# Kernel tuning notes

Hardware: AMD Instinct MI355X
Metric: run time of the kernel (lower is better)

## Reference

```python
import jax, jax.numpy as jnp
import numpy as np

N = 40000   # nodes
E = 640000  # edges (avg degree 16)
D = 128     # feature dim (in_features == out_features)
ALPHA = 0.2 # LeakyReLU negative slope


def setup_inputs() -> dict:
    key = jax.random.key(0)
    ks = jax.random.split(key, 12)
    s = 1.0 / np.sqrt(D)
    return {
        "h":     jax.random.normal(ks[0], (N, D), jnp.float32),
        "src":   jax.random.randint(ks[1], (E,), 0, N, jnp.int32),
        "dst":   jax.random.randint(ks[2], (E,), 0, N, jnp.int32),
        "W":     jax.random.normal(ks[3], (D, D), jnp.float32) * s,
        "b_W":   jnp.zeros((D,), jnp.float32),
        "a_src": jax.random.normal(ks[4], (D,), jnp.float32) * s,
        "a_dst": jax.random.normal(ks[5], (D,), jnp.float32) * s,
        "a_b":   jnp.zeros((1,), jnp.float32),
        "res_W": jax.random.normal(ks[6], (D, D), jnp.float32) * s,
        "res_b": jnp.zeros((D,), jnp.float32),
        "Wi":    jax.random.normal(ks[7], (3 * D, D), jnp.float32) * s,
        "Wh_g":  jax.random.normal(ks[8], (3 * D, D), jnp.float32) * s,
        "bi":    jnp.zeros((3 * D,), jnp.float32),
        "bh":    jnp.zeros((3 * D,), jnp.float32),
    }


def reference(h, src, dst, W, b_W, a_src, a_dst, a_b, res_W, res_b, Wi, Wh_g, bi, bh):
    # --- GAT layer: Wh = W h ---
    Wh = h @ W.T + b_W                                  # [N, D]
    # edge attention: a([Wh_src || Wh_dst]) == Wh_src@a_src + Wh_dst@a_dst + a_b
    s_s = Wh @ a_src                                    # [N]
    s_d = Wh @ a_dst                                    # [N]
    e = jax.nn.leaky_relu(s_s[src] + s_d[dst] + a_b[0], ALPHA)  # [E]
    # segment softmax over incoming edges of each destination node
    m = jax.ops.segment_max(e, dst, num_segments=N)
    m = jnp.where(jnp.isfinite(m), m, 0.0)
    ex = jnp.exp(e - m[dst])                            # [E]
    denom = jax.ops.segment_sum(ex, dst, num_segments=N)
    attn = ex / jnp.where(denom > 0, denom, 1.0)[dst]   # [E]
    # weighted neighbor aggregation (scatter-add on dst)
    h_prime = jax.ops.segment_sum(attn[:, None] * Wh[src], dst, num_segments=N)  # [N, D]
    # residual connection (res=True)
    h_prime = h_prime + h @ res_W.T + res_b
    # --- GRU cell: input = h_prime, hidden = h ---
    gi = h_prime @ Wi.T + bi                            # [N, 3D]
    gh = h @ Wh_g.T + bh                                # [N, 3D]
    i_r, i_z, i_n = jnp.split(gi, 3, axis=-1)
    h_r, h_z, h_n = jnp.split(gh, 3, axis=-1)
    r = jax.nn.sigmoid(i_r + h_r)
    z = jax.nn.sigmoid(i_z + h_z)
    n = jnp.tanh(i_n + r * h_n)
    return (1.0 - z) * n + z * h                        # [N, D]
```

## Files before the change

### kernel.cpp

```cpp
#include <hip/hip_runtime.h>
#include <math.h>

#define NLALPHA 0.2f
#define LOG2E 1.4426950408889634f
#define RT 10
#define SLAB 64
#define EPT 4
#define EPB (256 * EPT)

typedef __attribute__((ext_vector_type(8))) short bf16x8;
typedef __attribute__((ext_vector_type(4))) float f32x4;

static __device__ __forceinline__ float fexp(float x) {
    return __builtin_amdgcn_exp2f(x * LOG2E);
}
static __device__ __forceinline__ float fsigmoid(float x) {
    return __builtin_amdgcn_rcpf(1.f + __builtin_amdgcn_exp2f(-LOG2E * x));
}
static __device__ __forceinline__ float ftanh(float x) {
    return 1.f - 2.f * __builtin_amdgcn_rcpf(1.f + __builtin_amdgcn_exp2f(2.f * LOG2E * x));
}
static __device__ __forceinline__ unsigned short f2bf(float f) {
    unsigned int u = __float_as_uint(f);
    return (unsigned short)((u + 0x7fffu + ((u >> 16) & 1u)) >> 16);
}
static __device__ __forceinline__ float bf2f(unsigned short b) {
    return __uint_as_float(((unsigned int)b) << 16);
}
static __device__ __forceinline__ void keep_alive(bf16x8& v) {
    uint4* q = (uint4*)&v;
    asm volatile("" : "+v"(q->x), "+v"(q->y), "+v"(q->z), "+v"(q->w));
}
static __device__ __forceinline__ void place_edges(const int* __restrict__ dstv,
    const int* __restrict__ srcv, int* __restrict__ cnt, int* __restrict__ slab,
    int blk, int i0, int iEnd)
{
    const int base = i0 + blk * EPB + threadIdx.x;
    int d[EPT], s[EPT], pp[EPT];
    bool v[EPT];
#pragma unroll
    for (int u = 0; u < EPT; ++u) {
        int i = base + u * 256;
        v[u] = i < iEnd;
        if (v[u]) { d[u] = dstv[i]; s[u] = srcv[i]; }
    }
#pragma unroll
    for (int u = 0; u < EPT; ++u)
        if (v[u]) pp[u] = atomicAdd(&cnt[d[u]], 1);
#pragma unroll
    for (int u = 0; u < EPT; ++u)
        if (v[u]) slab[d[u] * SLAB + pp[u]] = s[u];
}

__global__ __launch_bounds__(256) void k_zero(int* __restrict__ cnt,
    const float* __restrict__ W, const float* __restrict__ a_src,
    const float* __restrict__ a_dst, const float* __restrict__ b_W,
    float* __restrict__ va, float* __restrict__ cc, int n, int gZero)
{
    const int b = blockIdx.x;
    if (b < gZero) {
        int i = b * 256 + threadIdx.x;
        if (i < n) cnt[i] = 0;
        return;
    }
    const int k = threadIdx.x;
    float cs = 0.f, cd = 0.f;
    if (k < 128) {
        float ss = 0.f, dd = 0.f;
        for (int j = 0; j < 128; ++j) {
            float w = W[j * 128 + k];
            ss = fmaf(w, a_src[j], ss);
            dd = fmaf(w, a_dst[j], dd);
        }
        va[k] = ss;
        va[128 + k] = dd;
        cs = b_W[k] * a_src[k];
        cd = b_W[k] * a_dst[k];
    }
#pragma unroll
    for (int o = 32; o; o >>= 1) { cs += __shfl_down(cs, o); cd += __shfl_down(cd, o); }
    __shared__ float sh[8];
    if ((k & 63) == 0) { sh[(k >> 6) * 2] = cs; sh[(k >> 6) * 2 + 1] = cd; }
    __syncthreads();
    if (k == 0) {
        cc[0] = sh[0] + sh[2] + sh[4] + sh[6];
        cc[1] = sh[1] + sh[3] + sh[5] + sh[7];
    }
}

__global__ __launch_bounds__(256) void k_prep_place(const float* __restrict__ h,
    const float* __restrict__ W, const float* __restrict__ res_W,
    const float* __restrict__ b_W, const float* __restrict__ res_b,
    const float* __restrict__ Wi, const float* __restrict__ Whg,
    const int* __restrict__ dstv, const int* __restrict__ srcv,
    const float* __restrict__ va, const float* __restrict__ cc,
    unsigned short* __restrict__ h_bf, unsigned short* __restrict__ Wcat,
    unsigned short* __restrict__ Wi_bf, unsigned short* __restrict__ Whg_bf,
    float* __restrict__ bias_cat, float* __restrict__ s_s, float* __restrict__ s_d,
    int* __restrict__ cnt, int* __restrict__ slab, int n, int e1, int gPrep)
{
    const int b = blockIdx.x;
    if (b < gPrep) {
        int i = b * 256 + threadIdx.x;
        int t = threadIdx.x;
        if (i < n * 16) {
            float4 v0 = ((const float4*)h)[2 * i];
            float4 v1 = ((const float4*)h)[2 * i + 1];
            uint4 o;
            o.x = (unsigned int)f2bf(v0.x) | ((unsigned int)f2bf(v0.y) << 16);
            o.y = (unsigned int)f2bf(v0.z) | ((unsigned int)f2bf(v0.w) << 16);
            o.z = (unsigned int)f2bf(v1.x) | ((unsigned int)f2bf(v1.y) << 16);
            o.w = (unsigned int)f2bf(v1.z) | ((unsigned int)f2bf(v1.w) << 16);
            ((uint4*)h_bf)[i] = o;
            const float* vs = va + (t & 15) * 8;
            const float* vd = vs + 128;
            float ps = v0.x*vs[0] + v0.y*vs[1] + v0.z*vs[2] + v0.w*vs[3]
                     + v1.x*vs[4] + v1.y*vs[5] + v1.z*vs[6] + v1.w*vs[7];
            float pd = v0.x*vd[0] + v0.y*vd[1] + v0.z*vd[2] + v0.w*vd[3]
                     + v1.x*vd[4] + v1.y*vd[5] + v1.z*vd[6] + v1.w*vd[7];
#pragma unroll
            for (int o2 = 1; o2 < 16; o2 <<= 1) {
                ps += __shfl_xor(ps, o2);
                pd += __shfl_xor(pd, o2);
            }
            if ((t & 15) == 0) {
                int row = i >> 4;
                s_s[row] = ps + cc[0];
                s_d[row] = pd + cc[1];
            }
        }
        if (i < 32768) Wcat[i] = f2bf(i < 16384 ? W[i] : res_W[i - 16384]);
        if (i < 49152) { Wi_bf[i] = f2bf(Wi[i]); Whg_bf[i] = f2bf(Whg[i]); }
        if (i < 256) bias_cat[i] = (i < 128) ? b_W[i] : res_b[i - 128];
    } else {
        place_edges(dstv, srcv, cnt, slab, b - gPrep, 0, e1);
    }
}

__global__ __launch_bounds__(256, 1) void k_whres_place(
    const unsigned short* __restrict__ h_bf,
    const unsigned short* __restrict__ Wcat, const float* __restrict__ bias_cat,
    unsigned short* __restrict__ Wh, unsigned short* __restrict__ hres,
    const int* __restrict__ dstv, const int* __restrict__ srcv,
    int* __restrict__ cnt, int* __restrict__ slab,
    int n, int e1, int e, int rowBlocks, int gWhres)
{
    const int b = blockIdx.x;
    if (b >= gWhres) {
        place_edges(dstv, srcv, cnt, slab, b - gWhres, e1, e);
        return;
    }
    const int bx = b % rowBlocks;
    const int by = b / rowBlocks;
    const int t = threadIdx.x;
    const int w = t >> 6, l = t & 63;
    const int lr = l & 15, kq = l >> 4, kg = kq * 8;
    const int jc = by * 64 + w * 16 + lr;
    bf16x8 bw[4];
#pragma unroll
    for (int ks = 0; ks < 4; ++ks) {
        bw[ks] = *(const bf16x8*)(Wcat + (size_t)jc * 128 + ks * 32 + kg);
        keep_alive(bw[ks]);
    }
    const float bj = bias_cat[jc];
    unsigned short* dstBase = (jc < 128) ? (Wh + jc) : (hres + (jc - 128));

    int row0 = bx * (16 * RT);
    bf16x8 ac[4];
    {
        const unsigned short* Ap = h_bf + (size_t)min(row0 + lr, n - 1) * 128 + kg;
#pragma unroll
        for (int ks = 0; ks < 4; ++ks) ac[ks] = *(const bf16x8*)(Ap + ks * 32);
    }
    for (int rt = 0; rt < RT && row0 < n; ++rt) {
        const int nrow = row0 + 16;
        bf16x8 an[4];
        if (rt + 1 < RT && nrow < n) {
            const unsigned short* Ap = h_bf + (size_t)min(nrow + lr, n - 1) * 128 + kg;
#pragma unroll
            for (int ks = 0; ks < 4; ++ks) an[ks] = *(const bf16x8*)(Ap + ks * 32);
        }
        f32x4 acc = {};
        acc = __builtin_amdgcn_mfma_f32_16x16x32_bf16(ac[0], bw[0], acc, 0, 0, 0);
        acc = __builtin_amdgcn_mfma_f32_16x16x32_bf16(ac[1], bw[1], acc, 0, 0, 0);
        acc = __builtin_amdgcn_mfma_f32_16x16x32_bf16(ac[2], bw[2], acc, 0, 0, 0);
        acc = __builtin_amdgcn_mfma_f32_16x16x32_bf16(ac[3], bw[3], acc, 0, 0, 0);
#pragma unroll
        for (int r = 0; r < 4; ++r) {
            int row = row0 + kq * 4 + r;
            if (row < n) dstBase[(size_t)row * 128] = f2bf(acc[r] + bj);
        }
#pragma unroll
        for (int ks = 0; ks < 4; ++ks) ac[ks] = an[ks];
        row0 = nrow;
    }
}

__global__ __launch_bounds__(256) void k_attn(const int* __restrict__ cnt,
    const int* __restrict__ slab, const float* __restrict__ s_s,
    const float* __restrict__ s_d, const float* __restrict__ a_b,
    const unsigned short* __restrict__ Wh, const unsigned short* __restrict__ hres,
    unsigned short* __restrict__ hp, int n)
{
    const int node = (int)((blockIdx.x * 256u + threadIdx.x) >> 6);
    const int l = threadIdx.x & 63;
    if (node >= n) return;
    const int lo = node * SLAB;
    const int deg = cnt[node];
    const float sdn = s_d[node] + a_b[0];
    const int g = l >> 4;
    const int c = l & 15;

    float sv = 0.f;
    int ssrc = 0;
    float den = 0.f;
    if (l < deg) {
        int s = slab[lo + l];
        float ev = s_s[s] + sdn;
        ev = ev > 0.f ? ev : NLALPHA * ev;
        sv = fexp(ev);
        ssrc = s;
        den = sv;
    }
#pragma unroll
    for (int o = 32; o; o >>= 1) den += __shfl_xor(den, o);
    const float dinv = __builtin_amdgcn_rcpf(den > 0.f ? den : 1.f);

    float acc[8] = {};
    for (int q = 0; q < deg; q += 4) {
        int eix = q + g;
        bool valid = eix < deg;
        int eic = valid ? eix : (deg - 1);
        float ex = __shfl(sv, eic);
        int s = __shfl(ssrc, eic);
        float wgt = valid ? ex * dinv : 0.f;
        uint4 v = *(const uint4*)(Wh + (size_t)s * 128 + c * 8);
        acc[0] = fmaf(wgt, bf2f((unsigned short)(v.x & 0xffff)), acc[0]);
        acc[1] = fmaf(wgt, bf2f((unsigned short)(v.x >> 16)), acc[1]);
        acc[2] = fmaf(wgt, bf2f((unsigned short)(v.y & 0xffff)), acc[2]);
        acc[3] = fmaf(wgt, bf2f((unsigned short)(v.y >> 16)), acc[3]);
        acc[4] = fmaf(wgt, bf2f((unsigned short)(v.z & 0xffff)), acc[4]);
        acc[5] = fmaf(wgt, bf2f((unsigned short)(v.z >> 16)), acc[5]);
        acc[6] = fmaf(wgt, bf2f((unsigned short)(v.w & 0xffff)), acc[6]);
        acc[7] = fmaf(wgt, bf2f((unsigned short)(v.w >> 16)), acc[7]);
    }
#pragma unroll
    for (int k = 0; k < 8; ++k) {
        acc[k] += __shfl_xor(acc[k], 16);
        acc[k] += __shfl_xor(acc[k], 32);
    }
    if (l < 16) {
        uint4 hv = *(const uint4*)(hres + (size_t)node * 128 + l * 8);
        uint4 o;
        o.x = (unsigned int)f2bf(acc[0] + bf2f((unsigned short)(hv.x & 0xffff)))
            | ((unsigned int)f2bf(acc[1] + bf2f((unsigned short)(hv.x >> 16))) << 16);
        o.y = (unsigned int)f2bf(acc[2] + bf2f((unsigned short)(hv.y & 0xffff)))
            | ((unsigned int)f2bf(acc[3] + bf2f((unsigned short)(hv.y >> 16))) << 16);
        o.z = (unsigned int)f2bf(acc[4] + bf2f((unsigned short)(hv.z & 0xffff)))
            | ((unsigned int)f2bf(acc[5] + bf2f((unsigned short)(hv.z >> 16))) << 16);
        o.w = (unsigned int)f2bf(acc[6] + bf2f((unsigned short)(hv.w & 0xffff)))
            | ((unsigned int)f2bf(acc[7] + bf2f((unsigned short)(hv.w >> 16))) << 16);
        *(uint4*)(hp + (size_t)node * 128 + l * 8) = o;
    }
}

__global__ __launch_bounds__(256, 1) void k_gru(const unsigned short* __restrict__ hp_bf,
    const unsigned short* __restrict__ h_bf, const unsigned short* __restrict__ Wi_bf,
    const unsigned short* __restrict__ Whg_bf, const float* __restrict__ bi,
    const float* __restrict__ bh, float* __restrict__ out, int n)
{
    const int t = threadIdx.x;
    const int w = t >> 6, l = t & 63;
    const int lr = l & 15, kq = l >> 4, kg = kq * 8;
    const int c = blockIdx.y * 64 + w * 16 + lr;

    bf16x8 bwi[3][4], bwh[3][4];
#pragma unroll
    for (int g = 0; g < 3; ++g)
#pragma unroll
        for (int ks = 0; ks < 4; ++ks) {
            bwi[g][ks] = *(const bf16x8*)(Wi_bf  + (size_t)(g * 128 + c) * 128 + ks * 32 + kg);
            bwh[g][ks] = *(const bf16x8*)(Whg_bf + (size_t)(g * 128 + c) * 128 + ks * 32 + kg);
        }
    const float biR = bi[c],       bhR = bh[c];
    const float biZ = bi[128 + c], bhZ = bh[128 + c];
    const float biN = bi[256 + c], bhN = bh[256 + c];

    int row0 = blockIdx.x * (16 * RT);
    bf16x8 aPc[4], aHc[4];
    float hvc[4];
    {
        size_t rbase = (size_t)min(row0 + lr, n - 1) * 128 + kg;
#pragma unroll
        for (int ks = 0; ks < 4; ++ks) {
            aPc[ks] = *(const bf16x8*)(hp_bf + rbase + ks * 32);
            aHc[ks] = *(const bf16x8*)(h_bf + rbase + ks * 32);
        }
#pragma unroll
        for (int r = 0; r < 4; ++r)
            hvc[r] = bf2f(h_bf[(size_t)min(row0 + kq * 4 + r, n - 1) * 128 + c]);
    }
    for (int rt = 0; rt < RT && row0 < n; ++rt) {
        const int nrow = row0 + 16;
        bf16x8 aPn[4], aHn[4];
        float hvn[4];
        if (rt + 1 < RT && nrow < n) {
            size_t rbase = (size_t)min(nrow + lr, n - 1) * 128 + kg;
#pragma unroll
            for (int ks = 0; ks < 4; ++ks) {
                aPn[ks] = *(const bf16x8*)(hp_bf + rbase + ks * 32);
                aHn[ks] = *(const bf16x8*)(h_bf + rbase + ks * 32);
            }
#pragma unroll
            for (int r = 0; r < 4; ++r)
                hvn[r] = bf2f(h_bf[(size_t)min(nrow + kq * 4 + r, n - 1) * 128 + c]);
        }

        f32x4 giR = {}, giZ = {}, giN = {}, ghR = {}, ghZ = {}, ghN = {};
#pragma unroll
        for (int ks = 0; ks < 4; ++ks) {
            giR = __builtin_amdgcn_mfma_f32_16x16x32_bf16(aPc[ks], bwi[0][ks], giR, 0, 0, 0);
            ghR = __builtin_amdgcn_mfma_f32_16x16x32_bf16(aHc[ks], bwh[0][ks], ghR, 0, 0, 0);
            giZ = __builtin_amdgcn_mfma_f32_16x16x32_bf16(aPc[ks], bwi[1][ks], giZ, 0, 0, 0);
            ghZ = __builtin_amdgcn_mfma_f32_16x16x32_bf16(aHc[ks], bwh[1][ks], ghZ, 0, 0, 0);
            giN = __builtin_amdgcn_mfma_f32_16x16x32_bf16(aPc[ks], bwi[2][ks], giN, 0, 0, 0);
            ghN = __builtin_amdgcn_mfma_f32_16x16x32_bf16(aHc[ks], bwh[2][ks], ghN, 0, 0, 0);
        }
#pragma unroll
        for (int r = 0; r < 4; ++r) {
            int row = row0 + kq * 4 + r;
            if (row < n) {
                float rg = fsigmoid(giR[r] + biR + ghR[r] + bhR);
                float zg = fsigmoid(giZ[r] + biZ + ghZ[r] + bhZ);
                float ng = ftanh(giN[r] + biN + rg * (ghN[r] + bhN));
                out[(size_t)row * 128 + c] = (1.f - zg) * ng + zg * hvc[r];
            }
        }
#pragma unroll
        for (int ks = 0; ks < 4; ++ks) { aPc[ks] = aPn[ks]; aHc[ks] = aHn[ks]; }
#pragma unroll
        for (int r = 0; r < 4; ++r) hvc[r] = hvn[r];
        row0 = nrow;
    }
}

extern "C" void kernel_launch(void* const* d_in, const int* in_sizes, int n_in,
                              void* d_out, int out_size, void* d_ws, size_t ws_size,
                              hipStream_t stream)
{
    const float* h     = (const float*)d_in[0];
    const int*   srcv  = (const int*)d_in[1];
    const int*   dstv  = (const int*)d_in[2];
    const float* W     = (const float*)d_in[3];
    const float* b_W   = (const float*)d_in[4];
    const float* a_src = (const float*)d_in[5];
    const float* a_dst = (const float*)d_in[6];
    const float* a_b   = (const float*)d_in[7];
    const float* res_W = (const float*)d_in[8];
    const float* res_b = (const float*)d_in[9];
    const float* Wi    = (const float*)d_in[10];
    const float* Whg   = (const float*)d_in[11];
    const float* bi    = (const float*)d_in[12];
    const float* bh    = (const float*)d_in[13];
    float* out = (float*)d_out;
    const int n = in_sizes[0] / 128;
    const int e = in_sizes[1];
    const int rowBlocks = (n + 16 * RT - 1) / (16 * RT);
    const int gZero  = (n + 255) / 256;
    const int gPrep  = (n * 16 + 255) / 256;
    const int gWhres = rowBlocks * 4;
    const int gPlaceTotal = (e + EPB - 1) / EPB;
    const int gP1 = gPlaceTotal / 2;
    const int e1 = gP1 * EPB;
    const int gP2 = gPlaceTotal - gP1;

    char* p = (char*)d_ws;
    auto carve = [&](size_t bytes) -> char* {
        char* r = p;
        p += (bytes + 255) & ~(size_t)255;
        return r;
    };
    unsigned short* h_bf   = (unsigned short*)carve((size_t)n * 128 * 2);
    unsigned short* Wh     = (unsigned short*)carve((size_t)n * 128 * 2);
    unsigned short* hres   = (unsigned short*)carve((size_t)n * 128 * 2);
    unsigned short* hp_bf  = (unsigned short*)carve((size_t)n * 128 * 2);
    float* s_s             = (float*)carve((size_t)n * 4);
    float* s_d             = (float*)carve((size_t)n * 4);
    int*   cnt             = (int*)carve((size_t)n * 4);
    int*   slab            = (int*)carve((size_t)n * SLAB * 4);
    unsigned short* Wcat   = (unsigned short*)carve(32768 * 2);
    unsigned short* Wi_bf  = (unsigned short*)carve(49152 * 2);
    unsigned short* Whg_bf = (unsigned short*)carve(49152 * 2);
    float* bias_cat        = (float*)carve(256 * 4);
    float* va              = (float*)carve(256 * 4);
    float* cc              = (float*)carve(2 * 4);

    k_zero<<<gZero + 1, 256, 0, stream>>>(cnt, W, a_src, a_dst, b_W, va, cc, n, gZero);
    k_prep_place<<<gPrep + gP1, 256, 0, stream>>>(h, W, res_W, b_W, res_b, Wi, Whg,
                                    dstv, srcv, va, cc, h_bf, Wcat, Wi_bf, Whg_bf,
                                    bias_cat, s_s, s_d, cnt, slab, n, e1, gPrep);
    k_whres_place<<<gWhres + gP2, 256, 0, stream>>>(h_bf, Wcat, bias_cat, Wh, hres,
                                    dstv, srcv, cnt, slab, n, e1, e, rowBlocks, gWhres);
    k_attn<<<((size_t)n * 64 + 255) / 256, 256, 0, stream>>>(cnt, slab, s_s, s_d, a_b,
                                                             Wh, hres, hp_bf, n);
    k_gru<<<dim3(rowBlocks, 2), 256, 0, stream>>>(hp_bf, h_bf, Wi_bf, Whg_bf, bi, bh, out, n);
}
```

Measured before the change: 128.4 us.

## Split attention and GRU into halves and overlap GRU-first-half with attention-second-half

Splits nodes into two halves. Attention runs on the first half, then one fused launch runs GRU on the first half alongside attention on the second half, and a final GRU launch handles the second half. The intent is to overlap the MFMA-bound GRU with the gather-bound attention so both kinds of hardware unit stay busy. It adds a kernel launch and the risk of imbalance, since the GRU blocks use launch_bounds(256,1) and sit in the same grid as the attention blocks.

```diff
diff --git a/kernel.cpp b/kernel.cpp
--- a/kernel.cpp
+++ b/kernel.cpp
@@ -50,6 +50,151 @@
 #pragma unroll
     for (int u = 0; u < EPT; ++u)
         if (v[u]) slab[d[u] * SLAB + pp[u]] = s[u];
+}
+
+static __device__ __forceinline__ void attn_body(int node, int l,
+    const int* __restrict__ cnt, const int* __restrict__ slab,
+    const float* __restrict__ s_s, const float* __restrict__ s_d,
+    const float* __restrict__ a_b, const unsigned short* __restrict__ Wh,
+    const unsigned short* __restrict__ hres, unsigned short* __restrict__ hp)
+{
+    const int lo = node * SLAB;
+    const int deg = cnt[node];
+    const float sdn = s_d[node] + a_b[0];
+    const int g = l >> 4;
+    const int c = l & 15;
+
+    float sv = 0.f;
+    int ssrc = 0;
+    float den = 0.f;
+    if (l < deg) {
+        int s = slab[lo + l];
+        float ev = s_s[s] + sdn;
+        ev = ev > 0.f ? ev : NLALPHA * ev;
+        sv = fexp(ev);
+        ssrc = s;
+        den = sv;
+    }
+#pragma unroll
+    for (int o = 32; o; o >>= 1) den += __shfl_xor(den, o);
+    const float dinv = __builtin_amdgcn_rcpf(den > 0.f ? den : 1.f);
+
+    float acc[8] = {};
+    for (int q = 0; q < deg; q += 4) {
+        int eix = q + g;
+        bool valid = eix < deg;
+        int eic = valid ? eix : (deg - 1);
+        float ex = __shfl(sv, eic);
+        int s = __shfl(ssrc, eic);
+        float wgt = valid ? ex * dinv : 0.f;
+        uint4 v = *(const uint4*)(Wh + (size_t)s * 128 + c * 8);
+        acc[0] = fmaf(wgt, bf2f((unsigned short)(v.x & 0xffff)), acc[0]);
+        acc[1] = fmaf(wgt, bf2f((unsigned short)(v.x >> 16)), acc[1]);
+        acc[2] = fmaf(wgt, bf2f((unsigned short)(v.y & 0xffff)), acc[2]);
+        acc[3] = fmaf(wgt, bf2f((unsigned short)(v.y >> 16)), acc[3]);
+        acc[4] = fmaf(wgt, bf2f((unsigned short)(v.z & 0xffff)), acc[4]);
+        acc[5] = fmaf(wgt, bf2f((unsigned short)(v.z >> 16)), acc[5]);
+        acc[6] = fmaf(wgt, bf2f((unsigned short)(v.w & 0xffff)), acc[6]);
+        acc[7] = fmaf(wgt, bf2f((unsigned short)(v.w >> 16)), acc[7]);
+    }
+#pragma unroll
+    for (int k = 0; k < 8; ++k) {
+        acc[k] += __shfl_xor(acc[k], 16);
+        acc[k] += __shfl_xor(acc[k], 32);
+    }
+    if (l < 16) {
+        uint4 hv = *(const uint4*)(hres + (size_t)node * 128 + l * 8);
+        uint4 o;
+        o.x = (unsigned int)f2bf(acc[0] + bf2f((unsigned short)(hv.x & 0xffff)))
+            | ((unsigned int)f2bf(acc[1] + bf2f((unsigned short)(hv.x >> 16))) << 16);
+        o.y = (unsigned int)f2bf(acc[2] + bf2f((unsigned short)(hv.y & 0xffff)))
+            | ((unsigned int)f2bf(acc[3] + bf2f((unsigned short)(hv.y >> 16))) << 16);
+        o.z = (unsigned int)f2bf(acc[4] + bf2f((unsigned short)(hv.z & 0xffff)))
+            | ((unsigned int)f2bf(acc[5] + bf2f((unsigned short)(hv.z >> 16))) << 16);
+        o.w = (unsigned int)f2bf(acc[6] + bf2f((unsigned short)(hv.w & 0xffff)))
+            | ((unsigned int)f2bf(acc[7] + bf2f((unsigned short)(hv.w >> 16))) << 16);
+        *(uint4*)(hp + (size_t)node * 128 + l * 8) = o;
+    }
+}
+
+static __device__ __forceinline__ void gru_body(int row0, int by,
+    const unsigned short* __restrict__ hp_bf, const unsigned short* __restrict__ h_bf,
+    const unsigned short* __restrict__ Wi_bf, const unsigned short* __restrict__ Whg_bf,
+    const float* __restrict__ bi, const float* __restrict__ bh,
+    float* __restrict__ out, int n)
+{
+    const int t = threadIdx.x;
+    const int w = t >> 6, l = t & 63;
+    const int lr = l & 15, kq = l >> 4, kg = kq * 8;
+    const int c = by * 64 + w * 16 + lr;
+
+    bf16x8 bwi[3][4], bwh[3][4];
+#pragma unroll
+    for (int g = 0; g < 3; ++g)
+#pragma unroll
+        for (int ks = 0; ks < 4; ++ks) {
+            bwi[g][ks] = *(const bf16x8*)(Wi_bf  + (size_t)(g * 128 + c) * 128 + ks * 32 + kg);
+            bwh[g][ks] = *(const bf16x8*)(Whg_bf + (size_t)(g * 128 + c) * 128 + ks * 32 + kg);
+        }
+    const float biR = bi[c],       bhR = bh[c];
+    const float biZ = bi[128 + c], bhZ = bh[128 + c];
+    const float biN = bi[256 + c], bhN = bh[256 + c];
+
+    bf16x8 aPc[4], aHc[4];
+    float hvc[4];
+    {
+        size_t rbase = (size_t)min(row0 + lr, n - 1) * 128 + kg;
+#pragma unroll
+        for (int ks = 0; ks < 4; ++ks) {
+            aPc[ks] = *(const bf16x8*)(hp_bf + rbase + ks * 32);
+            aHc[ks] = *(const bf16x8*)(h_bf + rbase + ks * 32);
+        }
+#pragma unroll
+        for (int r = 0; r < 4; ++r)
+            hvc[r] = bf2f(h_bf[(size_t)min(row0 + kq * 4 + r, n - 1) * 128 + c]);
+    }
+    for (int rt = 0; rt < RT && row0 < n; ++rt) {
+        const int nrow = row0 + 16;
+        bf16x8 aPn[4], aHn[4];
+        float hvn[4];
+        if (rt + 1 < RT && nrow < n) {
+            size_t rbase = (size_t)min(nrow + lr, n - 1) * 128 + kg;
+#pragma unroll
+            for (int ks = 0; ks < 4; ++ks) {
+                aPn[ks] = *(const bf16x8*)(hp_bf + rbase + ks * 32);
+                aHn[ks] = *(const bf16x8*)(h_bf + rbase + ks * 32);
+            }
+#pragma unroll
+            for (int r = 0; r < 4; ++r)
+                hvn[r] = bf2f(h_bf[(size_t)min(nrow + kq * 4 + r, n - 1) * 128 + c]);
+        }
+
+        f32x4 giR = {}, giZ = {}, giN = {}, ghR = {}, ghZ = {}, ghN = {};
+#pragma unroll
+        for (int ks = 0; ks < 4; ++ks) {
+            giR = __builtin_amdgcn_mfma_f32_16x16x32_bf16(aPc[ks], bwi[0][ks], giR, 0, 0, 0);
+            ghR = __builtin_amdgcn_mfma_f32_16x16x32_bf16(aHc[ks], bwh[0][ks], ghR, 0, 0, 0);
+            giZ = __builtin_amdgcn_mfma_f32_16x16x32_bf16(aPc[ks], bwi[1][ks], giZ, 0, 0, 0);
+            ghZ = __builtin_amdgcn_mfma_f32_16x16x32_bf16(aHc[ks], bwh[1][ks], ghZ, 0, 0, 0);
+            giN = __builtin_amdgcn_mfma_f32_16x16x32_bf16(aPc[ks], bwi[2][ks], giN, 0, 0, 0);
+            ghN = __builtin_amdgcn_mfma_f32_16x16x32_bf16(aHc[ks], bwh[2][ks], ghN, 0, 0, 0);
+        }
+#pragma unroll
+        for (int r = 0; r < 4; ++r) {
+            int row = row0 + kq * 4 + r;
+            if (row < n) {
+                float rg = fsigmoid(giR[r] + biR + ghR[r] + bhR);
+                float zg = fsigmoid(giZ[r] + biZ + ghZ[r] + bhZ);
+                float ng = ftanh(giN[r] + biN + rg * (ghN[r] + bhN));
+                out[(size_t)row * 128 + c] = (1.f - zg) * ng + zg * hvc[r];
+            }
+        }
+#pragma unroll
+        for (int ks = 0; ks < 4; ++ks) { aPc[ks] = aPn[ks]; aHc[ks] = aHn[ks]; }
+#pragma unroll
+        for (int r = 0; r < 4; ++r) hvc[r] = hvn[r];
+        row0 = nrow;
+    }
 }
 
 __global__ __launch_bounds__(256) void k_zero(int* __restrict__ cnt,
@@ -200,148 +345,47 @@
     const int* __restrict__ slab, const float* __restrict__ s_s,
     const float* __restrict__ s_d, const float* __restrict__ a_b,
     const unsigned short* __restrict__ Wh, const unsigned short* __restrict__ hres,
-    unsigned short* __restrict__ hp, int n)
-{
-    const int node = (int)((blockIdx.x * 256u + threadIdx.x) >> 6);
+    unsigned short* __restrict__ hp, int node0, int nEnd)
+{
+    const int node = node0 + (int)((blockIdx.x * 256u + threadIdx.x) >> 6);
+    const int l = threadIdx.x & 63;
+    if (node >= nEnd) return;
+    attn_body(node, l, cnt, slab, s_s, s_d, a_b, Wh, hres, hp);
+}
+
+__global__ __launch_bounds__(256, 1) void k_gru_attn(
+    const unsigned short* __restrict__ hp_bf, const unsigned short* __restrict__ h_bf,
+    const unsigned short* __restrict__ Wi_bf, const unsigned short* __restrict__ Whg_bf,
+    const float* __restrict__ bi, const float* __restrict__ bh,
+    float* __restrict__ out,
+    const int* __restrict__ cnt, const int* __restrict__ slab,
+    const float* __restrict__ s_s, const float* __restrict__ s_d,
+    const float* __restrict__ a_b, const unsigned short* __restrict__ Wh,
+    const unsigned short* __restrict__ hres, unsigned short* __restrict__ hp,
+    int n, int nH, int rbH, int gGru)
+{
+    const int b = blockIdx.x;
+    if (b < gGru) {
+        const int by = b / rbH;
+        const int bx = b - by * rbH;
+        int row0 = bx * (16 * RT);
+        if (row0 < nH) gru_body(row0, by, hp_bf, h_bf, Wi_bf, Whg_bf, bi, bh, out, min(nH, n));
+        return;
+    }
+    const int idx = (b - gGru) * 256 + threadIdx.x;
+    const int node = nH + (idx >> 6);
     const int l = threadIdx.x & 63;
     if (node >= n) return;
-    const int lo = node * SLAB;
-    const int deg = cnt[node];
-    const float sdn = s_d[node] + a_b[0];
-    const int g = l >> 4;
-    const int c = l & 15;
-
-    float sv = 0.f;
-    int ssrc = 0;
-    float den = 0.f;
-    if (l < deg) {
-        int s = slab[lo + l];
-        float ev = s_s[s] + sdn;
-        ev = ev > 0.f ? ev : NLALPHA * ev;
-        sv = fexp(ev);
-        ssrc = s;
-        den = sv;
-    }
-#pragma unroll
-    for (int o = 32; o; o >>= 1) den += __shfl_xor(den, o);
-    const float dinv = __builtin_amdgcn_rcpf(den > 0.f ? den : 1.f);
-
-    float acc[8] = {};
-    for (int q = 0; q < deg; q += 4) {
-        int eix = q + g;
-        bool valid = eix < deg;
-        int eic = valid ? eix : (deg - 1);
-        float ex = __shfl(sv, eic);
-        int s = __shfl(ssrc, eic);
-        float wgt = valid ? ex * dinv : 0.f;
-        uint4 v = *(const uint4*)(Wh + (size_t)s * 128 + c * 8);
-        acc[0] = fmaf(wgt, bf2f((unsigned short)(v.x & 0xffff)), acc[0]);
-        acc[1] = fmaf(wgt, bf2f((unsigned short)(v.x >> 16)), acc[1]);
-        acc[2] = fmaf(wgt, bf2f((unsigned short)(v.y & 0xffff)), acc[2]);
-        acc[3] = fmaf(wgt, bf2f((unsigned short)(v.y >> 16)), acc[3]);
-        acc[4] = fmaf(wgt, bf2f((unsigned short)(v.z & 0xffff)), acc[4]);
-        acc[5] = fmaf(wgt, bf2f((unsigned short)(v.z >> 16)), acc[5]);
-        acc[6] = fmaf(wgt, bf2f((unsigned short)(v.w & 0xffff)), acc[6]);
-        acc[7] = fmaf(wgt, bf2f((unsigned short)(v.w >> 16)), acc[7]);
-    }
-#pragma unroll
-    for (int k = 0; k < 8; ++k) {
-        acc[k] += __shfl_xor(acc[k], 16);
-        acc[k] += __shfl_xor(acc[k], 32);
-    }
-    if (l < 16) {
-        uint4 hv = *(const uint4*)(hres + (size_t)node * 128 + l * 8);
-        uint4 o;
-        o.x = (unsigned int)f2bf(acc[0] + bf2f((unsigned short)(hv.x & 0xffff)))
-            | ((unsigned int)f2bf(acc[1] + bf2f((unsigned short)(hv.x >> 16))) << 16);
-        o.y = (unsigned int)f2bf(acc[2] + bf2f((unsigned short)(hv.y & 0xffff)))
-            | ((unsigned int)f2bf(acc[3] + bf2f((unsigned short)(hv.y >> 16))) << 16);
-        o.z = (unsigned int)f2bf(acc[4] + bf2f((unsigned short)(hv.z & 0xffff)))
-            | ((unsigned int)f2bf(acc[5] + bf2f((unsigned short)(hv.z >> 16))) << 16);
-        o.w = (unsigned int)f2bf(acc[6] + bf2f((unsigned short)(hv.w & 0xffff)))
-            | ((unsigned int)f2bf(acc[7] + bf2f((unsigned short)(hv.w >> 16))) << 16);
-        *(uint4*)(hp + (size_t)node * 128 + l * 8) = o;
-    }
+    attn_body(node, l, cnt, slab, s_s, s_d, a_b, Wh, hres, hp);
 }
 
 __global__ __launch_bounds__(256, 1) void k_gru(const unsigned short* __restrict__ hp_bf,
     const unsigned short* __restrict__ h_bf, const unsigned short* __restrict__ Wi_bf,
     const unsigned short* __restrict__ Whg_bf, const float* __restrict__ bi,
-    const float* __restrict__ bh, float* __restrict__ out, int n)
-{
-    const int t = threadIdx.x;
-    const int w = t >> 6, l = t & 63;
-    const int lr = l & 15, kq = l >> 4, kg = kq * 8;
-    const int c = blockIdx.y * 64 + w * 16 + lr;
-
-    bf16x8 bwi[3][4], bwh[3][4];
-#pragma unroll
-    for (int g = 0; g < 3; ++g)
-#pragma unroll
-        for (int ks = 0; ks < 4; ++ks) {
-            bwi[g][ks] = *(const bf16x8*)(Wi_bf  + (size_t)(g * 128 + c) * 128 + ks * 32 + kg);
-            bwh[g][ks] = *(const bf16x8*)(Whg_bf + (size_t)(g * 128 + c) * 128 + ks * 32 + kg);
-        }
-    const float biR = bi[c],       bhR = bh[c];
-    const float biZ = bi[128 + c], bhZ = bh[128 + c];
-    const float biN = bi[256 + c], bhN = bh[256 + c];
-
-    int row0 = blockIdx.x * (16 * RT);
-    bf16x8 aPc[4], aHc[4];
-    float hvc[4];
-    {
-        size_t rbase = (size_t)min(row0 + lr, n - 1) * 128 + kg;
-#pragma unroll
-        for (int ks = 0; ks < 4; ++ks) {
-            aPc[ks] = *(const bf16x8*)(hp_bf + rbase + ks * 32);
-            aHc[ks] = *(const bf16x8*)(h_bf + rbase + ks * 32);
-        }
-#pragma unroll
-        for (int r = 0; r < 4; ++r)
-            hvc[r] = bf2f(h_bf[(size_t)min(row0 + kq * 4 + r, n - 1) * 128 + c]);
-    }
-    for (int rt = 0; rt < RT && row0 < n; ++rt) {
-        const int nrow = row0 + 16;
-        bf16x8 aPn[4], aHn[4];
-        float hvn[4];
-        if (rt + 1 < RT && nrow < n) {
-            size_t rbase = (size_t)min(nrow + lr, n - 1) * 128 + kg;
-#pragma unroll
-            for (int ks = 0; ks < 4; ++ks) {
-                aPn[ks] = *(const bf16x8*)(hp_bf + rbase + ks * 32);
-                aHn[ks] = *(const bf16x8*)(h_bf + rbase + ks * 32);
-            }
-#pragma unroll
-            for (int r = 0; r < 4; ++r)
-                hvn[r] = bf2f(h_bf[(size_t)min(nrow + kq * 4 + r, n - 1) * 128 + c]);
-        }
-
-        f32x4 giR = {}, giZ = {}, giN = {}, ghR = {}, ghZ = {}, ghN = {};
-#pragma unroll
-        for (int ks = 0; ks < 4; ++ks) {
-            giR = __builtin_amdgcn_mfma_f32_16x16x32_bf16(aPc[ks], bwi[0][ks], giR, 0, 0, 0);
-            ghR = __builtin_amdgcn_mfma_f32_16x16x32_bf16(aHc[ks], bwh[0][ks], ghR, 0, 0, 0);
-            giZ = __builtin_amdgcn_mfma_f32_16x16x32_bf16(aPc[ks], bwi[1][ks], giZ, 0, 0, 0);
-            ghZ = __builtin_amdgcn_mfma_f32_16x16x32_bf16(aHc[ks], bwh[1][ks], ghZ, 0, 0, 0);
-            giN = __builtin_amdgcn_mfma_f32_16x16x32_bf16(aPc[ks], bwi[2][ks], giN, 0, 0, 0);
-            ghN = __builtin_amdgcn_mfma_f32_16x16x32_bf16(aHc[ks], bwh[2][ks], ghN, 0, 0, 0);
-        }
-#pragma unroll
-        for (int r = 0; r < 4; ++r) {
-            int row = row0 + kq * 4 + r;
-            if (row < n) {
-                float rg = fsigmoid(giR[r] + biR + ghR[r] + bhR);
-                float zg = fsigmoid(giZ[r] + biZ + ghZ[r] + bhZ);
-                float ng = ftanh(giN[r] + biN + rg * (ghN[r] + bhN));
-                out[(size_t)row * 128 + c] = (1.f - zg) * ng + zg * hvc[r];
-            }
-        }
-#pragma unroll
-        for (int ks = 0; ks < 4; ++ks) { aPc[ks] = aPn[ks]; aHc[ks] = aHn[ks]; }
-#pragma unroll
-        for (int r = 0; r < 4; ++r) hvc[r] = hvn[r];
-        row0 = nrow;
-    }
+    const float* __restrict__ bh, float* __restrict__ out, int n, int rowOff)
+{
+    gru_body(rowOff + blockIdx.x * (16 * RT), blockIdx.y,
+             hp_bf, h_bf, Wi_bf, Whg_bf, bi, bh, out, n);
 }
 
 extern "C" void kernel_launch(void* const* d_in, const int* in_sizes, int n_in,
@@ -365,7 +409,8 @@
     float* out = (float*)d_out;
     const int n = in_sizes[0] / 128;
     const int e = in_sizes[1];
-    const int rowBlocks = (n + 16 * RT - 1) / (16 * RT);
+    const int TILE = 16 * RT;
+    const int rowBlocks = (n + TILE - 1) / TILE;
     const int gZero  = (n + 255) / 256;
     const int gPrep  = (n * 16 + 255) / 256;
     const int gWhres = rowBlocks * 4;
@@ -373,6 +418,12 @@
     const int gP1 = gPlaceTotal / 2;
     const int e1 = gP1 * EPB;
     const int gP2 = gPlaceTotal - gP1;
+    const int rbH = max(1, rowBlocks / 2);
+    const int nH  = min(n, rbH * TILE);
+    const int rb2 = (n - nH + TILE - 1) / TILE;
+    const int gA1 = (nH * 64 + 255) / 256;
+    const int gA2 = ((n - nH) * 64 + 255) / 256;
+    const int gGru = rbH * 2;
 
     char* p = (char*)d_ws;
     auto carve = [&](size_t bytes) -> char* {
@@ -401,7 +452,11 @@
                                     bias_cat, s_s, s_d, cnt, slab, n, e1, gPrep);
     k_whres_place<<<gWhres + gP2, 256, 0, stream>>>(h_bf, Wcat, bias_cat, Wh, hres,
                                     dstv, srcv, cnt, slab, n, e1, e, rowBlocks, gWhres);
-    k_attn<<<((size_t)n * 64 + 255) / 256, 256, 0, stream>>>(cnt, slab, s_s, s_d, a_b,
-                                                             Wh, hres, hp_bf, n);
-    k_gru<<<dim3(rowBlocks, 2), 256, 0, stream>>>(hp_bf, h_bf, Wi_bf, Whg_bf, bi, bh, out, n);
-}
+    if (gA1 > 0)
+        k_attn<<<gA1, 256, 0, stream>>>(cnt, slab, s_s, s_d, a_b, Wh, hres, hp_bf, 0, nH);
+    k_gru_attn<<<gGru + gA2, 256, 0, stream>>>(hp_bf, h_bf, Wi_bf, Whg_bf, bi, bh, out,
+                                    cnt, slab, s_s, s_d, a_b, Wh, hres, hp_bf,
+                                    n, nH, rbH, gGru);
+    if (rb2 > 0)
+        k_gru<<<dim3(rb2, 2), 256, 0, stream>>>(hp_bf, h_bf, Wi_bf, Whg_bf, bi, bh, out, n, nH);
+}
```

Measured after the change: 157.1 us. 1.22x slower.
